# Optimization experiments

Hardware: AMD Instinct MI355X
Metric: run time of the kernel (lower is better)

The kernel has to match this reference:

```python
import jax, jax.numpy as jnp
import numpy as np

D_MODEL = 1024
D_STATE = 16
D_CONV = 4
EXPAND = 2
D_INNER = EXPAND * D_MODEL          # 2048
DT_RANK = (D_MODEL + 15) // 16      # 64
IN_SIZE = 512
OUT_SIZE = 512
BATCH = 2048


def setup_inputs() -> dict:
    key = jax.random.key(0)
    ks = jax.random.split(key, 12)
    s = lambda k, shape, sc=0.02: jax.random.normal(k, shape, dtype=jnp.float32) * sc
    return {
        "x": jax.random.normal(ks[0], (1, BATCH, IN_SIZE), dtype=jnp.float32),
        "rnn_states": jax.random.normal(ks[1], (1, BATCH, D_INNER * (D_CONV + D_STATE)), dtype=jnp.float32),
        # CustomMamba projections (nn.Linear stored as (in, out) so we do x @ W + b)
        "w_inp": s(ks[2], (IN_SIZE, D_MODEL)),
        "b_inp": jnp.zeros((D_MODEL,), jnp.float32),
        "w_outp": s(ks[3], (D_MODEL, OUT_SIZE)),
        "b_outp": jnp.zeros((OUT_SIZE,), jnp.float32),
        # OrigMamba params (mamba_ssm layout, torch Linear weights as (out, in))
        "in_proj_w": s(ks[4], (2 * D_INNER, D_MODEL)),
        "conv_w": s(ks[5], (D_INNER, D_CONV), 0.1),   # conv1d.weight squeezed over channel dim
        "conv_b": jnp.zeros((D_INNER,), jnp.float32),
        "x_proj_w": s(ks[6], (DT_RANK + 2 * D_STATE, D_INNER)),
        "dt_proj_w": s(ks[7], (D_INNER, DT_RANK), 0.1),
        "dt_proj_b": s(ks[8], (D_INNER,), 0.5),
        "A_log": jnp.log(jnp.tile(jnp.arange(1, D_STATE + 1, dtype=jnp.float32), (D_INNER, 1))),
        "D": jnp.ones((D_INNER,), jnp.float32),
        "out_proj_w": s(ks[9], (D_MODEL, D_INNER)),
    }


def reference(x, rnn_states, w_inp, b_inp, w_outp, b_outp,
              in_proj_w, conv_w, conv_b, x_proj_w, dt_proj_w, dt_proj_b,
              A_log, D, out_proj_w):
    B = rnn_states.shape[1]
    # unpack recurrent state: (B, d_inner, d_conv + d_state)
    rs = rnn_states.reshape(B, D_INNER, D_CONV + D_STATE)
    conv_state = rs[..., :D_CONV]          # (B, d_inner, d_conv)
    ssm_state = rs[..., D_CONV:]           # (B, d_inner, d_state)

    # input projection; seqlen==1 (step path of Mamba), drop the time dim
    h = x[0] @ w_inp + b_inp               # (B, d_model)

    # ---- Mamba single-token step ----
    xz = h @ in_proj_w.T                   # (B, 2*d_inner)
    xi, z = xz[:, :D_INNER], xz[:, D_INNER:]

    # shift conv window left, append new token
    conv_state = jnp.concatenate([conv_state[..., 1:], xi[..., None]], axis=-1)
    xc = jax.nn.silu(jnp.sum(conv_state * conv_w, axis=-1) + conv_b)  # (B, d_inner)

    xdb = xc @ x_proj_w.T                  # (B, dt_rank + 2*d_state)
    dt = jax.nn.softplus(xdb[:, :DT_RANK] @ dt_proj_w.T + dt_proj_b)  # (B, d_inner)
    Bm = xdb[:, DT_RANK:DT_RANK + D_STATE]  # (B, d_state)
    Cm = xdb[:, DT_RANK + D_STATE:]         # (B, d_state)

    A = -jnp.exp(A_log)                    # (d_inner, d_state)
    dA = jnp.exp(dt[:, :, None] * A[None])                 # (B, d_inner, d_state)
    ssm_state = ssm_state * dA + (dt * xc)[:, :, None] * Bm[:, None, :]

    y = jnp.einsum('bdn,bn->bd', ssm_state, Cm) + D * xc
    y = y * jax.nn.silu(z)
    core_out = y @ out_proj_w.T            # (B, d_model)

    out = (core_out @ w_outp + b_outp)[None]  # (1, B, output_size)
    new_rnn_states = jnp.concatenate([conv_state, ssm_state], axis=-1).reshape(B, -1)
    return out, new_rnn_states
```

## Files before the change

### kernel.cpp

```cpp
#include <hip/hip_runtime.h>
#include <math.h>


#define BATCH 2048
#define D_INNER 2048
#define D_STATE 16
#define D_CONV 4
#define DT_RANK 64
#define XDB_N 96
#define RNN_ROW 40960

typedef unsigned short u16;
typedef short bf16x8 __attribute__((ext_vector_type(8)));
typedef float f32x4 __attribute__((ext_vector_type(4)));

__device__ __forceinline__ float silu_f(float v) {
    return v / (1.f + __expf(-v));
}

__device__ __forceinline__ u16 f2bf(float x) {
    unsigned int u = __float_as_uint(x);
    u += 0x7FFFu + ((u >> 16) & 1u);
    return (u16)(u >> 16);
}
__device__ __forceinline__ float bf2f(u16 b) {
    return __uint_as_float(((unsigned int)b) << 16);
}
__device__ __forceinline__ void split_f(float x, u16& h, u16& l) {
    h = f2bf(x);
    l = f2bf(x - bf2f(h));
}

typedef __attribute__((address_space(1))) const unsigned int guint;
typedef __attribute__((address_space(3))) unsigned int luint;
__device__ __forceinline__ void gload16(const void* g, void* l) {
    __builtin_amdgcn_global_load_lds((guint*)g, (luint*)l, 16, 0, 0);
}

template<bool BIAS, bool SPLITOUT>
__global__ __launch_bounds__(256)
void gemm_mfma(const u16* __restrict__ Ah, const u16* __restrict__ Al,
               const u16* __restrict__ Bh, const u16* __restrict__ Bl,
               const float* __restrict__ bias,
               float* __restrict__ Cf, u16* __restrict__ Ch, u16* __restrict__ Cl,
               int M, int N, int K) {
    __shared__ u16 sA_h[2][128 * 32];
    __shared__ u16 sA_l[2][128 * 32];
    __shared__ u16 sB_h[2][128 * 32];
    __shared__ u16 sB_l[2][128 * 32];

    const int tid  = threadIdx.x;
    const int wave = tid >> 6;
    const int lane = tid & 63;
    const int l16  = lane & 15;
    const int lsel = lane >> 4;

    int bx = blockIdx.x, by = blockIdx.y;
    {
        const int gx = gridDim.x;
        const int nwg = gx * gridDim.y;
        int bid = by * gx + bx;
        if ((nwg & 7) == 0) {
            bid = (bid & 7) * (nwg >> 3) + (bid >> 3);
            bx = bid % gx;
            by = bid / gx;
        }
    }
    const int m0 = by * 128;
    const int n0 = bx * 128;

    const int c0 = tid, c1 = tid + 256;
    const int sr0 = c0 >> 2, ss0 = ((c0 & 3) ^ ((sr0 >> 1) & 3)) * 8;
    const int sr1 = c1 >> 2, ss1 = ((c1 & 3) ^ ((sr1 >> 1) & 3)) * 8;
    const u16* gA0h = Ah + (size_t)(m0 + sr0) * K + ss0;
    const u16* gA1h = Ah + (size_t)(m0 + sr1) * K + ss1;
    const u16* gA0l = Al + (size_t)(m0 + sr0) * K + ss0;
    const u16* gA1l = Al + (size_t)(m0 + sr1) * K + ss1;
    const u16* gB0h = Bh + (size_t)(n0 + sr0) * K + ss0;
    const u16* gB1h = Bh + (size_t)(n0 + sr1) * K + ss1;
    const u16* gB0l = Bl + (size_t)(n0 + sr0) * K + ss0;
    const u16* gB1l = Bl + (size_t)(n0 + sr1) * K + ss1;
    const int l0 = c0 * 8, l1 = c1 * 8;

    const int arow = (wave >> 1) * 64 + l16;
    const int brow = (wave & 1) * 64 + l16;
    const int swz  = (lsel ^ ((l16 >> 1) & 3)) * 8;

    f32x4 acc[4][4];
#pragma unroll
    for (int i = 0; i < 4; ++i)
#pragma unroll
        for (int j = 0; j < 4; ++j) acc[i][j] = f32x4{0.f, 0.f, 0.f, 0.f};

    auto stage = [&](int buf, int k0) {
        gload16(gA0h + k0, &sA_h[buf][l0]);
        gload16(gA1h + k0, &sA_h[buf][l1]);
        gload16(gA0l + k0, &sA_l[buf][l0]);
        gload16(gA1l + k0, &sA_l[buf][l1]);
        gload16(gB0h + k0, &sB_h[buf][l0]);
        gload16(gB1h + k0, &sB_h[buf][l1]);
        gload16(gB0l + k0, &sB_l[buf][l0]);
        gload16(gB1l + k0, &sB_l[buf][l1]);
    };

    int cur = 0;
    stage(0, 0);
    for (int k0 = 0; k0 < K; k0 += 32) {
        __syncthreads();
        if (k0 + 32 < K) stage(cur ^ 1, k0 + 32);

        bf16x8 bh[4], bl[4];
#pragma unroll
        for (int j = 0; j < 4; ++j) {
            bh[j] = *(const bf16x8*)&sB_h[cur][(brow + j * 16) * 32 + swz];
            bl[j] = *(const bf16x8*)&sB_l[cur][(brow + j * 16) * 32 + swz];
        }
#pragma unroll
        for (int i = 0; i < 4; ++i) {
            bf16x8 ah = *(const bf16x8*)&sA_h[cur][(arow + i * 16) * 32 + swz];
            bf16x8 al = *(const bf16x8*)&sA_l[cur][(arow + i * 16) * 32 + swz];
#pragma unroll
            for (int j = 0; j < 4; ++j) {
                acc[i][j] = __builtin_amdgcn_mfma_f32_16x16x32_bf16(ah, bh[j], acc[i][j], 0, 0, 0);
                acc[i][j] = __builtin_amdgcn_mfma_f32_16x16x32_bf16(al, bh[j], acc[i][j], 0, 0, 0);
                acc[i][j] = __builtin_amdgcn_mfma_f32_16x16x32_bf16(ah, bl[j], acc[i][j], 0, 0, 0);
            }
        }
        cur ^= 1;
    }

    const int crow = m0 + (wave >> 1) * 64 + lsel * 4;
    const int ccol = n0 + (wave & 1) * 64 + l16;
#pragma unroll
    for (int i = 0; i < 4; ++i) {
#pragma unroll
        for (int j = 0; j < 4; ++j) {
            const int col = ccol + j * 16;
            float bv = 0.f;
            if (BIAS) bv = bias[col];
#pragma unroll
            for (int r = 0; r < 4; ++r) {
                const int row = crow + i * 16 + r;
                float v = acc[i][j][r] + bv;
                if (SPLITOUT) {
                    u16 hh, ll;
                    split_f(v, hh, ll);
                    Ch[(size_t)row * N + col] = hh;
                    Cl[(size_t)row * N + col] = ll;
                } else {
                    Cf[(size_t)row * N + col] = v;
                }
            }
        }
    }
}

__global__ __launch_bounds__(256)
void split_nt(const float* __restrict__ W, u16* __restrict__ H, u16* __restrict__ L, int n4) {
    const int i = blockIdx.x * 256 + threadIdx.x;
    if (i >= n4) return;
    float4 v = ((const float4*)W)[i];
    u16 h0, l0, h1, l1, h2, l2, h3, l3;
    split_f(v.x, h0, l0); split_f(v.y, h1, l1);
    split_f(v.z, h2, l2); split_f(v.w, h3, l3);
    ushort4 hv; hv.x = h0; hv.y = h1; hv.z = h2; hv.w = h3;
    ushort4 lv; lv.x = l0; lv.y = l1; lv.z = l2; lv.w = l3;
    *(ushort4*)&H[(size_t)i * 4] = hv;
    *(ushort4*)&L[(size_t)i * 4] = lv;
}

__global__ __launch_bounds__(256)
void split_t(const float* __restrict__ W, u16* __restrict__ H, u16* __restrict__ L,
             int K, int N) {
    __shared__ float t[32][33];
    const int n0 = blockIdx.x * 32;
    const int k0 = blockIdx.y * 32;
    const int tx = threadIdx.x & 31;
    const int ty = threadIdx.x >> 5;
#pragma unroll
    for (int s = 0; s < 32; s += 8)
        t[ty + s][tx] = W[(size_t)(k0 + ty + s) * N + n0 + tx];
    __syncthreads();
#pragma unroll
    for (int s = 0; s < 32; s += 8) {
        float v = t[tx][ty + s];
        u16 h, l;
        split_f(v, h, l);
        H[(size_t)(n0 + ty + s) * K + k0 + tx] = h;
        L[(size_t)(n0 + ty + s) * K + k0 + tx] = l;
    }
}

__global__ __launch_bounds__(256)
void conv_kernel(const float* __restrict__ rnn_in, const float* __restrict__ xz,
                 const float* __restrict__ conv_w, const float* __restrict__ conv_b,
                 float* __restrict__ xc) {
    __shared__ float row[5120];
    const int tid = threadIdx.x;
    const int b = blockIdx.y;
    const int d0 = blockIdx.x * 256;
    const float* src = rnn_in + (size_t)b * RNN_ROW + (size_t)d0 * 20;
#pragma unroll
    for (int i = 0; i < 5; ++i) {
        const int o = (i * 256 + tid) * 4;
        *(float4*)&row[o] = *(const float4*)&src[o];
    }
    __syncthreads();
    const int d = d0 + tid;
    const float c1 = row[tid * 20 + 1];
    const float c2 = row[tid * 20 + 2];
    const float c3 = row[tid * 20 + 3];
    const float xi = xz[(size_t)b * 4096 + d];
    const float4 w = *(const float4*)&conv_w[d * 4];
    const float pre = c1 * w.x + c2 * w.y + c3 * w.z + xi * w.w + conv_b[d];
    xc[(size_t)b * 2048 + d] = silu_f(pre);
}

__global__ __launch_bounds__(256)
void xproj_kernel(const float* __restrict__ xc, const float* __restrict__ xw,
                  float* __restrict__ xdb) {
    __shared__ float xsm[4096];
    const int tid = threadIdx.x;
    const int b0 = blockIdx.x * 2;
    const float* src = xc + (size_t)b0 * 2048;
#pragma unroll
    for (int i = 0; i < 4; ++i) {
        const int o = (i * 256 + tid) * 4;
        *(float4*)&xsm[o] = *(const float4*)&src[o];
    }
    __syncthreads();
    const int r = tid >> 7;
    const int n = tid & 127;
    if (n < XDB_N) {
        const float* xr = &xsm[r * 2048];
        const float* wr = &xw[(size_t)n * 2048];
        float acc = 0.f;
#pragma unroll 4
        for (int k = 0; k < 2048; k += 4) {
            float4 xv = *(const float4*)&xr[k];
            float4 w  = *(const float4*)&wr[k];
            acc = fmaf(xv.x, w.x, fmaf(xv.y, w.y, fmaf(xv.z, w.z, fmaf(xv.w, w.w, acc))));
        }
        xdb[(size_t)(b0 + r) * XDB_N + n] = acc;
    }
}

__global__ __launch_bounds__(256)
void ssm3_kernel(const float* __restrict__ rnn_in, const float* __restrict__ xdb,
                 const float* __restrict__ xc, const float* __restrict__ xz,
                 const float* __restrict__ dt_w, const float* __restrict__ dt_b,
                 const float* __restrict__ A_log, const float* __restrict__ Dp,
                 u16* __restrict__ y_h, u16* __restrict__ y_l,
                 float* __restrict__ rnn_out) {
    __shared__ float row[5120];
    __shared__ float xs[XDB_N];
    const int tid = threadIdx.x;
    const int b = blockIdx.y;
    const int d0 = blockIdx.x * 256;
    const int d = d0 + tid;
    const float* src = rnn_in + (size_t)b * RNN_ROW + (size_t)d0 * 20;
    float* dst = rnn_out + (size_t)b * RNN_ROW + (size_t)d0 * 20;

#pragma unroll
    for (int i = 0; i < 5; ++i) {
        const int o = (i * 256 + tid) * 4;
        *(float4*)&row[o] = *(const float4*)&src[o];
    }
    if (tid < XDB_N) xs[tid] = xdb[(size_t)b * XDB_N + tid];
    __syncthreads();

    float st[20];
#pragma unroll
    for (int i = 0; i < 20; ++i) st[i] = row[tid * 20 + i];

    float acc = dt_b[d];
#pragma unroll
    for (int k = 0; k < 64; k += 4) {
        float4 w = *(const float4*)&dt_w[(size_t)d * 64 + k];
        acc = fmaf(xs[k], w.x, fmaf(xs[k + 1], w.y,
              fmaf(xs[k + 2], w.z, fmaf(xs[k + 3], w.w, acc))));
    }
    const float dt = (acc > 20.f) ? acc : log1pf(__expf(acc));

    const float xc_v = xc[(size_t)b * 2048 + d];
    const float xi   = xz[(size_t)b * 4096 + d];
    const float z_v  = xz[(size_t)b * 4096 + 2048 + d];
    const float dtxc = dt * xc_v;

    float al[16];
    *(float4*)&al[0]  = *(const float4*)&A_log[(size_t)d * 16 + 0];
    *(float4*)&al[4]  = *(const float4*)&A_log[(size_t)d * 16 + 4];
    *(float4*)&al[8]  = *(const float4*)&A_log[(size_t)d * 16 + 8];
    *(float4*)&al[12] = *(const float4*)&A_log[(size_t)d * 16 + 12];

    float out[20];
    out[0] = st[1]; out[1] = st[2]; out[2] = st[3]; out[3] = xi;
    float y_acc = Dp[d] * xc_v;
#pragma unroll
    for (int s = 0; s < 16; ++s) {
        float ns = fmaf(st[4 + s], __expf(dt * -__expf(al[s])), dtxc * xs[DT_RANK + s]);
        out[4 + s] = ns;
        y_acc = fmaf(ns, xs[DT_RANK + 16 + s], y_acc);
    }

#pragma unroll
    for (int i = 0; i < 20; ++i) row[tid * 20 + i] = out[i];
    __syncthreads();

#pragma unroll
    for (int i = 0; i < 5; ++i) {
        const int o = (i * 256 + tid) * 4;
        *(float4*)&dst[o] = *(const float4*)&row[o];
    }

    const float yv = y_acc * silu_f(z_v);
    u16 hh, ll;
    split_f(yv, hh, ll);
    const size_t yo = (size_t)b * 2048 + d;
    y_h[yo] = hh;
    y_l[yo] = ll;
}

extern "C" void kernel_launch(void* const* d_in, const int* in_sizes, int n_in,
                              void* d_out, int out_size, void* d_ws, size_t ws_size,
                              hipStream_t stream) {
    const float* x         = (const float*)d_in[0];
    const float* rnn_in    = (const float*)d_in[1];
    const float* w_inp     = (const float*)d_in[2];
    const float* b_inp     = (const float*)d_in[3];
    const float* w_outp    = (const float*)d_in[4];
    const float* b_outp    = (const float*)d_in[5];
    const float* in_proj_w = (const float*)d_in[6];
    const float* conv_w    = (const float*)d_in[7];
    const float* conv_b    = (const float*)d_in[8];
    const float* x_proj_w  = (const float*)d_in[9];
    const float* dt_w      = (const float*)d_in[10];
    const float* dt_b      = (const float*)d_in[11];
    const float* A_log     = (const float*)d_in[12];
    const float* Dp        = (const float*)d_in[13];
    const float* out_proj_w= (const float*)d_in[14];

    float* out_main = (float*)d_out;
    float* rnn_out  = (float*)d_out + (size_t)BATCH * 512;

    float* ws = (float*)d_ws;
    float* xz     = ws;
    u16*   ip_h   = (u16*)(ws + 8388608);
    u16*   ip_l   = ip_h + 4194304;
    float* xc     = ws + 8388608;
    u16*   core_h = (u16*)(ws + 8388608);
    u16*   core_l = core_h + 2097152;
    u16*   h_h    = (u16*)(ws + 12582912);
    u16*   h_l    = h_h + 2097152;
    u16*   x_h    = (u16*)(ws + 14680064);
    u16*   x_l    = x_h + 1048576;
    u16*   wi_h   = (u16*)(ws + 15728640);
    u16*   wi_l   = wi_h + 524288;
    u16*   y_h    = (u16*)(ws + 12582912);
    u16*   y_l    = y_h + 4194304;
    u16*   op_h   = (u16*)(ws + 16777216);
    u16*   op_l   = op_h + 2097152;
    u16*   wo_h   = (u16*)(ws + 12582912);
    u16*   wo_l   = wo_h + 524288;
    float* xdb    = ws + 18874368;

    split_nt<<<1024, 256, 0, stream>>>(x, x_h, x_l, 262144);
    split_t <<<dim3(32, 16), 256, 0, stream>>>(w_inp, wi_h, wi_l, 512, 1024);
    split_nt<<<4096, 256, 0, stream>>>(in_proj_w, ip_h, ip_l, 1048576);
    split_nt<<<2048, 256, 0, stream>>>(out_proj_w, op_h, op_l, 524288);

    gemm_mfma<true, true><<<dim3(8, 16), 256, 0, stream>>>(
        x_h, x_l, wi_h, wi_l, b_inp, nullptr, h_h, h_l, BATCH, 1024, 512);
    gemm_mfma<false, false><<<dim3(32, 16), 256, 0, stream>>>(
        h_h, h_l, ip_h, ip_l, nullptr, xz, nullptr, nullptr, BATCH, 4096, 1024);
    conv_kernel<<<dim3(8, BATCH), 256, 0, stream>>>(
        rnn_in, xz, conv_w, conv_b, xc);
    xproj_kernel<<<BATCH / 2, 256, 0, stream>>>(xc, x_proj_w, xdb);
    ssm3_kernel<<<dim3(8, BATCH), 256, 0, stream>>>(
        rnn_in, xdb, xc, xz, dt_w, dt_b, A_log, Dp, y_h, y_l, rnn_out);
    gemm_mfma<false, true><<<dim3(8, 16), 256, 0, stream>>>(
        y_h, y_l, op_h, op_l, nullptr, nullptr, core_h, core_l, BATCH, 1024, 2048);
    split_t<<<dim3(16, 32), 256, 0, stream>>>(w_outp, wo_h, wo_l, 1024, 512);
    gemm_mfma<true, false><<<dim3(4, 16), 256, 0, stream>>>(
        core_h, core_l, wo_h, wo_l, b_outp, out_main, nullptr, nullptr, BATCH, 512, 1024);
}
```

Measured before the change: 1.192 ms.

## Fuse conv into x_proj kernel and batch SSM step with register-cached weights

Merges the depthwise conv and x_proj into one kernel that computes xc for four batch rows in shared memory and reduces each x_proj output with wave shuffles, removing the xc round trip through global memory. The SSM kernel now recomputes xc from the conv state itself, handles eight batch rows per block, keeps dt_proj weights, -exp(A_log) and conv parameters in registers across rows, and prefetches the next row's state while computing the current one. The conv-state columns 1-3 are read twice (once per kernel) and register pressure rises, with the launch bound capping occupancy at three blocks per SIMD.

```diff
diff --git a/kernel.cpp b/kernel.cpp
--- a/kernel.cpp
+++ b/kernel.cpp
@@ -192,133 +192,165 @@
 }
 
 __global__ __launch_bounds__(256)
-void conv_kernel(const float* __restrict__ rnn_in, const float* __restrict__ xz,
-                 const float* __restrict__ conv_w, const float* __restrict__ conv_b,
-                 float* __restrict__ xc) {
-    __shared__ float row[5120];
+void convproj_kernel(const float* __restrict__ rnn_in, const float* __restrict__ xz,
+                     const float* __restrict__ conv_w, const float* __restrict__ conv_b,
+                     const float* __restrict__ xw, float* __restrict__ xdb) {
+    __shared__ float xc[4][2048];
     const int tid = threadIdx.x;
-    const int b = blockIdx.y;
-    const int d0 = blockIdx.x * 256;
-    const float* src = rnn_in + (size_t)b * RNN_ROW + (size_t)d0 * 20;
-#pragma unroll
-    for (int i = 0; i < 5; ++i) {
-        const int o = (i * 256 + tid) * 4;
-        *(float4*)&row[o] = *(const float4*)&src[o];
+    const int b0 = blockIdx.x * 4;
+#pragma unroll
+    for (int bb = 0; bb < 4; ++bb) {
+        const int b = b0 + bb;
+#pragma unroll
+        for (int k = 0; k < 8; ++k) {
+            const int dd = k * 256 + tid;
+            float4 cs = *(const float4*)&rnn_in[(size_t)b * RNN_ROW + (size_t)dd * 20];
+            const float xi = xz[(size_t)b * 4096 + dd];
+            const float4 w = *(const float4*)&conv_w[dd * 4];
+            const float pre = cs.y * w.x + cs.z * w.y + cs.w * w.z + xi * w.w + conv_b[dd];
+            xc[bb][dd] = silu_f(pre);
+        }
     }
     __syncthreads();
-    const int d = d0 + tid;
-    const float c1 = row[tid * 20 + 1];
-    const float c2 = row[tid * 20 + 2];
-    const float c3 = row[tid * 20 + 3];
-    const float xi = xz[(size_t)b * 4096 + d];
-    const float4 w = *(const float4*)&conv_w[d * 4];
-    const float pre = c1 * w.x + c2 * w.y + c3 * w.z + xi * w.w + conv_b[d];
-    xc[(size_t)b * 2048 + d] = silu_f(pre);
-}
-
-__global__ __launch_bounds__(256)
-void xproj_kernel(const float* __restrict__ xc, const float* __restrict__ xw,
-                  float* __restrict__ xdb) {
-    __shared__ float xsm[4096];
-    const int tid = threadIdx.x;
-    const int b0 = blockIdx.x * 2;
-    const float* src = xc + (size_t)b0 * 2048;
-#pragma unroll
-    for (int i = 0; i < 4; ++i) {
-        const int o = (i * 256 + tid) * 4;
-        *(float4*)&xsm[o] = *(const float4*)&src[o];
-    }
-    __syncthreads();
-    const int r = tid >> 7;
-    const int n = tid & 127;
-    if (n < XDB_N) {
-        const float* xr = &xsm[r * 2048];
+    const int wave = tid >> 6;
+    const int lane = tid & 63;
+    for (int j = 0; j < 24; ++j) {
+        const int n = j * 4 + wave;
         const float* wr = &xw[(size_t)n * 2048];
-        float acc = 0.f;
-#pragma unroll 4
-        for (int k = 0; k < 2048; k += 4) {
-            float4 xv = *(const float4*)&xr[k];
-            float4 w  = *(const float4*)&wr[k];
-            acc = fmaf(xv.x, w.x, fmaf(xv.y, w.y, fmaf(xv.z, w.z, fmaf(xv.w, w.w, acc))));
-        }
-        xdb[(size_t)(b0 + r) * XDB_N + n] = acc;
-    }
-}
-
-__global__ __launch_bounds__(256)
-void ssm3_kernel(const float* __restrict__ rnn_in, const float* __restrict__ xdb,
-                 const float* __restrict__ xc, const float* __restrict__ xz,
+        float a0 = 0.f, a1 = 0.f, a2 = 0.f, a3 = 0.f;
+#pragma unroll
+        for (int it = 0; it < 8; ++it) {
+            const int k4 = (it * 64 + lane) * 4;
+            float4 wv = *(const float4*)&wr[k4];
+            float4 x0 = *(const float4*)&xc[0][k4];
+            float4 x1 = *(const float4*)&xc[1][k4];
+            float4 x2 = *(const float4*)&xc[2][k4];
+            float4 x3 = *(const float4*)&xc[3][k4];
+            a0 = fmaf(wv.x, x0.x, fmaf(wv.y, x0.y, fmaf(wv.z, x0.z, fmaf(wv.w, x0.w, a0))));
+            a1 = fmaf(wv.x, x1.x, fmaf(wv.y, x1.y, fmaf(wv.z, x1.z, fmaf(wv.w, x1.w, a1))));
+            a2 = fmaf(wv.x, x2.x, fmaf(wv.y, x2.y, fmaf(wv.z, x2.z, fmaf(wv.w, x2.w, a2))));
+            a3 = fmaf(wv.x, x3.x, fmaf(wv.y, x3.y, fmaf(wv.z, x3.z, fmaf(wv.w, x3.w, a3))));
+        }
+#pragma unroll
+        for (int m = 32; m > 0; m >>= 1) {
+            a0 += __shfl_xor(a0, m);
+            a1 += __shfl_xor(a1, m);
+            a2 += __shfl_xor(a2, m);
+            a3 += __shfl_xor(a3, m);
+        }
+        if (lane == 0) {
+            xdb[(size_t)(b0 + 0) * XDB_N + n] = a0;
+            xdb[(size_t)(b0 + 1) * XDB_N + n] = a1;
+            xdb[(size_t)(b0 + 2) * XDB_N + n] = a2;
+            xdb[(size_t)(b0 + 3) * XDB_N + n] = a3;
+        }
+    }
+}
+
+__global__ __launch_bounds__(256, 3)
+void ssm4_kernel(const float* __restrict__ rnn_in, const float* __restrict__ xdb,
+                 const float* __restrict__ xz,
                  const float* __restrict__ dt_w, const float* __restrict__ dt_b,
                  const float* __restrict__ A_log, const float* __restrict__ Dp,
+                 const float* __restrict__ conv_w, const float* __restrict__ conv_b,
                  u16* __restrict__ y_h, u16* __restrict__ y_l,
                  float* __restrict__ rnn_out) {
-    __shared__ float row[5120];
+    __shared__ float slab[5120];
     __shared__ float xs[XDB_N];
     const int tid = threadIdx.x;
-    const int b = blockIdx.y;
     const int d0 = blockIdx.x * 256;
-    const int d = d0 + tid;
-    const float* src = rnn_in + (size_t)b * RNN_ROW + (size_t)d0 * 20;
-    float* dst = rnn_out + (size_t)b * RNN_ROW + (size_t)d0 * 20;
-
-#pragma unroll
-    for (int i = 0; i < 5; ++i) {
-        const int o = (i * 256 + tid) * 4;
-        *(float4*)&row[o] = *(const float4*)&src[o];
-    }
-    if (tid < XDB_N) xs[tid] = xdb[(size_t)b * XDB_N + tid];
-    __syncthreads();
-
-    float st[20];
-#pragma unroll
-    for (int i = 0; i < 20; ++i) st[i] = row[tid * 20 + i];
-
-    float acc = dt_b[d];
-#pragma unroll
-    for (int k = 0; k < 64; k += 4) {
-        float4 w = *(const float4*)&dt_w[(size_t)d * 64 + k];
-        acc = fmaf(xs[k], w.x, fmaf(xs[k + 1], w.y,
-              fmaf(xs[k + 2], w.z, fmaf(xs[k + 3], w.w, acc))));
-    }
-    const float dt = (acc > 20.f) ? acc : log1pf(__expf(acc));
-
-    const float xc_v = xc[(size_t)b * 2048 + d];
-    const float xi   = xz[(size_t)b * 4096 + d];
-    const float z_v  = xz[(size_t)b * 4096 + 2048 + d];
-    const float dtxc = dt * xc_v;
-
-    float al[16];
-    *(float4*)&al[0]  = *(const float4*)&A_log[(size_t)d * 16 + 0];
-    *(float4*)&al[4]  = *(const float4*)&A_log[(size_t)d * 16 + 4];
-    *(float4*)&al[8]  = *(const float4*)&A_log[(size_t)d * 16 + 8];
-    *(float4*)&al[12] = *(const float4*)&A_log[(size_t)d * 16 + 12];
-
-    float out[20];
-    out[0] = st[1]; out[1] = st[2]; out[2] = st[3]; out[3] = xi;
-    float y_acc = Dp[d] * xc_v;
-#pragma unroll
-    for (int s = 0; s < 16; ++s) {
-        float ns = fmaf(st[4 + s], __expf(dt * -__expf(al[s])), dtxc * xs[DT_RANK + s]);
-        out[4 + s] = ns;
-        y_acc = fmaf(ns, xs[DT_RANK + 16 + s], y_acc);
-    }
-
-#pragma unroll
-    for (int i = 0; i < 20; ++i) row[tid * 20 + i] = out[i];
-    __syncthreads();
-
-#pragma unroll
-    for (int i = 0; i < 5; ++i) {
-        const int o = (i * 256 + tid) * 4;
-        *(float4*)&dst[o] = *(const float4*)&row[o];
-    }
-
-    const float yv = y_acc * silu_f(z_v);
-    u16 hh, ll;
-    split_f(yv, hh, ll);
-    const size_t yo = (size_t)b * 2048 + d;
-    y_h[yo] = hh;
-    y_l[yo] = ll;
+    const int b0 = blockIdx.y * 8;
+    const int d  = d0 + tid;
+
+    float4 wreg[16];
+#pragma unroll
+    for (int j = 0; j < 16; ++j)
+        wreg[j] = *(const float4*)&dt_w[(size_t)d * 64 + j * 4];
+    float A_row[16];
+    {
+        float al[16];
+        *(float4*)&al[0]  = *(const float4*)&A_log[(size_t)d * 16 + 0];
+        *(float4*)&al[4]  = *(const float4*)&A_log[(size_t)d * 16 + 4];
+        *(float4*)&al[8]  = *(const float4*)&A_log[(size_t)d * 16 + 8];
+        *(float4*)&al[12] = *(const float4*)&A_log[(size_t)d * 16 + 12];
+#pragma unroll
+        for (int s = 0; s < 16; ++s) A_row[s] = -__expf(al[s]);
+    }
+    const float4 cw  = *(const float4*)&conv_w[d * 4];
+    const float  cb  = conv_b[d];
+    const float  D_d = Dp[d];
+    const float  dtb = dt_b[d];
+
+    float4 rs[5];
+    {
+        const float* src = rnn_in + (size_t)b0 * RNN_ROW + (size_t)d0 * 20;
+#pragma unroll
+        for (int i = 0; i < 5; ++i) rs[i] = *(const float4*)&src[(i * 256 + tid) * 4];
+    }
+    float xv = 0.f;
+    if (tid < XDB_N) xv = xdb[(size_t)b0 * XDB_N + tid];
+
+    for (int g = 0; g < 8; ++g) {
+        const int b = b0 + g;
+        __syncthreads();
+#pragma unroll
+        for (int i = 0; i < 5; ++i) *(float4*)&slab[(i * 256 + tid) * 4] = rs[i];
+        if (tid < XDB_N) xs[tid] = xv;
+        __syncthreads();
+
+        const float xi = xz[(size_t)b * 4096 + d];
+        const float zv = xz[(size_t)b * 4096 + 2048 + d];
+        if (g < 7) {
+            const float* srcn = rnn_in + (size_t)(b + 1) * RNN_ROW + (size_t)d0 * 20;
+#pragma unroll
+            for (int i = 0; i < 5; ++i) rs[i] = *(const float4*)&srcn[(i * 256 + tid) * 4];
+            if (tid < XDB_N) xv = xdb[(size_t)(b + 1) * XDB_N + tid];
+        }
+
+        float st[20];
+#pragma unroll
+        for (int i = 0; i < 5; ++i)
+            *(float4*)&st[i * 4] = *(const float4*)&slab[tid * 20 + i * 4];
+
+        const float pre  = st[1] * cw.x + st[2] * cw.y + st[3] * cw.z + xi * cw.w + cb;
+        const float xc_v = silu_f(pre);
+
+        float acc = dtb;
+#pragma unroll
+        for (int j = 0; j < 16; ++j) {
+            acc = fmaf(xs[j * 4 + 0], wreg[j].x,
+                  fmaf(xs[j * 4 + 1], wreg[j].y,
+                  fmaf(xs[j * 4 + 2], wreg[j].z,
+                  fmaf(xs[j * 4 + 3], wreg[j].w, acc))));
+        }
+        const float dt   = (acc > 20.f) ? acc : log1pf(__expf(acc));
+        const float dtxc = dt * xc_v;
+
+        float y_acc = D_d * xc_v;
+#pragma unroll
+        for (int s = 0; s < 16; ++s) {
+            float ns = fmaf(st[4 + s], __expf(dt * A_row[s]), dtxc * xs[DT_RANK + s]);
+            st[4 + s] = ns;
+            y_acc = fmaf(ns, xs[DT_RANK + 16 + s], y_acc);
+        }
+        st[0] = st[1]; st[1] = st[2]; st[2] = st[3]; st[3] = xi;
+
+#pragma unroll
+        for (int i = 0; i < 5; ++i)
+            *(float4*)&slab[tid * 20 + i * 4] = *(const float4*)&st[i * 4];
+        __syncthreads();
+
+        float* dst = rnn_out + (size_t)b * RNN_ROW + (size_t)d0 * 20;
+#pragma unroll
+        for (int i = 0; i < 5; ++i)
+            *(float4*)&dst[(i * 256 + tid) * 4] = *(const float4*)&slab[(i * 256 + tid) * 4];
+
+        const float yv = y_acc * silu_f(zv);
+        u16 hh, ll;
+        split_f(yv, hh, ll);
+        y_h[(size_t)b * 2048 + d] = hh;
+        y_l[(size_t)b * 2048 + d] = ll;
+    }
 }
 
 extern "C" void kernel_launch(void* const* d_in, const int* in_sizes, int n_in,
@@ -347,7 +379,6 @@
     float* xz     = ws;
     u16*   ip_h   = (u16*)(ws + 8388608);
     u16*   ip_l   = ip_h + 4194304;
-    float* xc     = ws + 8388608;
     u16*   core_h = (u16*)(ws + 8388608);
     u16*   core_l = core_h + 2097152;
     u16*   h_h    = (u16*)(ws + 12582912);
@@ -373,11 +404,10 @@
         x_h, x_l, wi_h, wi_l, b_inp, nullptr, h_h, h_l, BATCH, 1024, 512);
     gemm_mfma<false, false><<<dim3(32, 16), 256, 0, stream>>>(
         h_h, h_l, ip_h, ip_l, nullptr, xz, nullptr, nullptr, BATCH, 4096, 1024);
-    conv_kernel<<<dim3(8, BATCH), 256, 0, stream>>>(
-        rnn_in, xz, conv_w, conv_b, xc);
-    xproj_kernel<<<BATCH / 2, 256, 0, stream>>>(xc, x_proj_w, xdb);
-    ssm3_kernel<<<dim3(8, BATCH), 256, 0, stream>>>(
-        rnn_in, xdb, xc, xz, dt_w, dt_b, A_log, Dp, y_h, y_l, rnn_out);
+    convproj_kernel<<<BATCH / 4, 256, 0, stream>>>(
+        rnn_in, xz, conv_w, conv_b, x_proj_w, xdb);
+    ssm4_kernel<<<dim3(8, BATCH / 8), 256, 0, stream>>>(
+        rnn_in, xdb, xz, dt_w, dt_b, A_log, Dp, conv_w, conv_b, y_h, y_l, rnn_out);
     gemm_mfma<false, true><<<dim3(8, 16), 256, 0, stream>>>(
         y_h, y_l, op_h, op_l, nullptr, nullptr, core_h, core_l, BATCH, 1024, 2048);
     split_t<<<dim3(16, 32), 256, 0, stream>>>(w_outp, wo_h, wo_l, 1024, 512);
```

Measured after the change: 1.004 ms. 1.19x faster.
